# Optimization experiments

Hardware: AMD Instinct MI355X
Metric: run time of the kernel (lower is better)

Reference implementation:

```python
import jax, jax.numpy as jnp
import numpy as np

NC, NG, D = 50000, 3000, 64
E_CG, E_GC, E_GG = 3_000_000, 3_000_000, 100_000
KEEP = 0.9  # 1 - drop_out


def _mask(key, n):
    return (jax.random.uniform(key, (n, 1)) < KEEP).astype(jnp.float32) / KEEP


def setup_inputs() -> dict:
    key = jax.random.key(0)
    ks = jax.random.split(key, 20)
    return {
        "c_feat": jax.random.normal(ks[0], (NC, D), jnp.float32),
        "g_feat": jax.random.normal(ks[1], (NG, D), jnp.float32),
        "cj_cell": jax.random.uniform(ks[2], (NC, 1), jnp.float32),
        "ci_cell": jax.random.uniform(ks[3], (NC, 1), jnp.float32),
        "cj_gene": jax.random.uniform(ks[4], (NG, 1), jnp.float32),
        "ci_gene": jax.random.uniform(ks[5], (NG, 1), jnp.float32),
        "cjj_gene": jax.random.uniform(ks[6], (NG, 1), jnp.float32),
        "cii_gene": jax.random.uniform(ks[7], (NG, 1), jnp.float32),
        "mask_exp": _mask(ks[8], NC),
        "mask_rev": _mask(ks[9], NG),
        "mask_gg": _mask(ks[10], NG),
        "src_cg": jax.random.randint(ks[11], (E_CG,), 0, NC, jnp.int32),
        "dst_cg": jax.random.randint(ks[12], (E_CG,), 0, NG, jnp.int32),
        "src_gc": jax.random.randint(ks[13], (E_GC,), 0, NG, jnp.int32),
        "dst_gc": jax.random.randint(ks[14], (E_GC,), 0, NC, jnp.int32),
        "src_gg": jax.random.randint(ks[15], (E_GG,), 0, NG, jnp.int32),
        "dst_gg": jax.random.randint(ks[16], (E_GG,), 0, NG, jnp.int32),
    }


def _light_conv(src_feats, cj, mask, ci, src, dst, n_dst):
    # weighted_feats = src_feats * dropout(cj); copy_u + sum; scale by ci
    wf = src_feats * (cj * mask)                      # [Nsrc, D]
    agg = jax.ops.segment_sum(wf[src], dst, num_segments=n_dst)  # [Ndst, D]
    return agg * ci


def reference(c_feat, g_feat, cj_cell, ci_cell, cj_gene, ci_gene,
              cjj_gene, cii_gene, mask_exp, mask_rev, mask_gg,
              src_cg, dst_cg, src_gc, dst_gc, src_gg, dst_gg):
    alpha1 = 0.5
    # relation 'exp': cell -> gene
    g_exp = _light_conv(c_feat, cj_cell, mask_exp, ci_gene, src_cg, dst_cg, NG)
    # relation 'reverse-exp': gene -> cell (only relation targeting cells)
    c_out = _light_conv(g_feat, cj_gene, mask_rev, ci_cell, src_gc, dst_gc, NC)
    # relation 'co-exp': gene -> gene (uses cjj/cii)
    g_gg = _light_conv(g_feat, cjj_gene, mask_gg, cii_gene, src_gg, dst_gg, NG)
    # aggregate='stack' over gene dst relations, then alpha-weighted combine
    g_out = alpha1 * g_exp + (1.0 - alpha1) * g_gg
    return (c_out, g_out)
```

## Files before the change

### kernel.cpp

```cpp
#include <hip/hip_runtime.h>

#define NC 50000
#define NG 3000
#define D  64

#define NB_CG 750
#define NB_GC 782
#define PBITS 18
#define TILE  8192
#define NPREP 128
#define CAP   4608
#define GG_CAP 128
#define OVF_CAP 262144

__device__ inline unsigned short f2bf(float x) {
    unsigned u = __float_as_uint(x);
    unsigned r = u + 0x7FFFu + ((u >> 16) & 1u);
    return (unsigned short)(r >> 16);
}

template <bool BF16>
__device__ inline void row8(const void* feat, int s, int l8, float f[8]) {
    if (BF16) {
        const uint4 q = *((const uint4*)((const unsigned short*)feat + (size_t)s * D) + l8);
        f[0] = __uint_as_float(q.x << 16); f[1] = __uint_as_float(q.x & 0xFFFF0000u);
        f[2] = __uint_as_float(q.y << 16); f[3] = __uint_as_float(q.y & 0xFFFF0000u);
        f[4] = __uint_as_float(q.z << 16); f[5] = __uint_as_float(q.z & 0xFFFF0000u);
        f[6] = __uint_as_float(q.w << 16); f[7] = __uint_as_float(q.w & 0xFFFF0000u);
    } else {
        const float4* row = (const float4*)((const float*)feat + (size_t)s * D);
        const float4 a = row[l8];
        const float4 b = row[l8 + 8];
        f[0] = a.x; f[1] = a.y; f[2] = a.z; f[3] = a.w;
        f[4] = b.x; f[5] = b.y; f[6] = b.z; f[7] = b.w;
    }
}


__global__ __launch_bounds__(256) void partition_kernel(
    const int* __restrict__ src_cg, const int* __restrict__ dst_cg, int e_cg, int nt_cg,
    const int* __restrict__ src_gc, const int* __restrict__ dst_gc, int e_gc, int nt_gc,
    const int* __restrict__ src_gg, const int* __restrict__ dst_gg, int e_gg,
    int* __restrict__ cur_cg, int* __restrict__ cur_gc, int* __restrict__ cnt_gg,
    unsigned* __restrict__ bkt_cg, unsigned* __restrict__ bkt_gc, int* __restrict__ bkt_gg,
    int* __restrict__ ovf_cnt, uint2* __restrict__ ovf,
    const float* __restrict__ cj_cell, const float* __restrict__ mask_exp,
    const float* __restrict__ cj_gene, const float* __restrict__ mask_rev,
    const float* __restrict__ cjj_gene, const float* __restrict__ mask_gg,
    float* __restrict__ w_cell, float* __restrict__ w_rev, float* __restrict__ w_gg,
    const float* __restrict__ c_feat, const float* __restrict__ g_feat,
    unsigned short* __restrict__ cf16, unsigned short* __restrict__ gf16, int do_cvt)
{
    const int tid = threadIdx.x;
    const int NT2 = nt_cg + nt_gc;

    if (blockIdx.x >= NT2 + 64) {
        const int pb = blockIdx.x - NT2 - 64;
        const long long stride = (long long)NPREP * 256;
        for (long long i = (long long)pb * 256 + tid; i < NC; i += stride)
            w_cell[i] = cj_cell[i] * mask_exp[i];
        for (long long i = (long long)pb * 256 + tid; i < NG; i += stride) {
            w_rev[i] = cj_gene[i] * mask_rev[i];
            w_gg[i]  = cjj_gene[i] * mask_gg[i];
        }
        if (do_cvt) {
            const long long total8 = (long long)(NC + NG) * D / 8;
            for (long long t = (long long)pb * 256 + tid; t < total8; t += stride) {
                const long long base = t * 8;
                const float* sp; unsigned short* dp;
                if (base < (long long)NC * D) { sp = c_feat + base; dp = cf16 + base; }
                else { sp = g_feat + (base - (long long)NC * D); dp = gf16 + (base - (long long)NC * D); }
                const float4 a = ((const float4*)sp)[0];
                const float4 b = ((const float4*)sp)[1];
                ((ushort4*)dp)[0] = make_ushort4(f2bf(a.x), f2bf(a.y), f2bf(a.z), f2bf(a.w));
                ((ushort4*)dp)[1] = make_ushort4(f2bf(b.x), f2bf(b.y), f2bf(b.z), f2bf(b.w));
            }
        }
        return;
    }

    if (blockIdx.x >= NT2) {
        for (long long e = (long long)(blockIdx.x - NT2) * 256 + tid; e < e_gg;
             e += (long long)64 * 256) {
            const int dd = dst_gg[e];
            const int ss = src_gg[e];
            if ((unsigned)dd >= (unsigned)NG || (unsigned)ss >= (unsigned)NG) continue;
            const int pos = atomicAdd(&cnt_gg[dd], 1);
            if (pos < GG_CAP) bkt_gg[dd * GG_CAP + pos] = ss;
            else {
                const int op = atomicAdd(ovf_cnt, 1);
                if (op >= 0 && op < OVF_CAP)
                    ovf[op] = make_uint2((2u << 30) | (unsigned)ss, (unsigned)dd);
            }
        }
        return;
    }

    const int* src; const int* dst; int ne; int* cur; unsigned* bkt;
    int shift, nbins, t; unsigned rel;
    if (blockIdx.x < nt_cg) { src = src_cg; dst = dst_cg; ne = e_cg; cur = cur_cg; bkt = bkt_cg; shift = 2; nbins = NB_CG; t = blockIdx.x;         rel = 0u; }
    else                    { src = src_gc; dst = dst_gc; ne = e_gc; cur = cur_gc; bkt = bkt_gc; shift = 6; nbins = NB_GC; t = blockIdx.x - nt_cg; rel = 1u; }
    const long long tb = (long long)t * TILE;
    if (tb >= ne) return;
    const int n = (int)((ne - tb) < TILE ? (ne - tb) : TILE);

    __shared__ int th[784];
    __shared__ int toff[784];
    __shared__ int tcur[784];
    __shared__ int gs[784];
    __shared__ unsigned staged[TILE];
    const unsigned PMASK = (1u << PBITS) - 1u;
    const unsigned DMASK = (1u << shift) - 1u;

    for (int i = tid; i < nbins; i += 256) { th[i] = 0; tcur[i] = 0; }
    __syncthreads();
    #pragma unroll 4
    for (int k = 0; k < TILE / 256; ++k) {
        int i = k * 256 + tid;
        if (i < n) {
            unsigned b = ((unsigned)dst[tb + i]) >> shift;
            if (b < (unsigned)nbins) atomicAdd(&th[b], 1);
        }
    }
    __syncthreads();
    if (tid < 64) {
        int carry = 0;
        for (int c = 0; c < nbins; c += 64) {
            int idx = c + tid;
            int v = (idx < nbins) ? th[idx] : 0;
            int incl = v;
            #pragma unroll
            for (int d = 1; d < 64; d <<= 1) {
                int x = __shfl_up(incl, d);
                if (tid >= d) incl += x;
            }
            if (idx < nbins) toff[idx] = incl - v + carry;
            carry += __shfl(incl, 63);
        }
    }
    __syncthreads();
    for (int i = tid; i < nbins; i += 256) {
        const int c = th[i];
        gs[i] = c ? atomicAdd(&cur[i], c) : 0;
    }
    __syncthreads();
    #pragma unroll 4
    for (int k = 0; k < TILE / 256; ++k) {
        int i = k * 256 + tid;
        if (i < n) {
            unsigned d = (unsigned)dst[tb + i];
            unsigned s = (unsigned)src[tb + i];
            unsigned b = d >> shift;
            if (b < (unsigned)nbins) {
                int p = toff[b] + atomicAdd(&tcur[b], 1);
                if (p >= 0 && p < TILE)
                    staged[p] = (b << PBITS) | (s << shift) | (d & DMASK);
            }
        }
    }
    __syncthreads();
    for (int i = tid; i < n; i += 256) {
        const unsigned v = staged[i];
        const unsigned b = v >> PBITS;
        const int local = gs[b] + (i - toff[b]);
        if (local < CAP) {
            bkt[(size_t)b * CAP + local] = v & PMASK;
        } else {
            const unsigned s = (v >> shift) & 0xFFFFu;
            const unsigned dd = (b << shift) | (v & DMASK);
            const int op = atomicAdd(ovf_cnt, 1);
            if (op >= 0 && op < OVF_CAP)
                ovf[op] = make_uint2((rel << 30) | s, dd);
        }
    }
}


template <bool BF16>
__global__ __launch_bounds__(256) void gather3_kernel(
    const unsigned* __restrict__ bkt_cg, const int* __restrict__ cur_cg,
    const unsigned* __restrict__ bkt_gc, const int* __restrict__ cur_gc,
    const void* __restrict__ cfeat, const void* __restrict__ gfeat,
    const float* __restrict__ w_cell, const float* __restrict__ w_rev, const float* __restrict__ w_gg,
    const float* __restrict__ ci_gene, const float* __restrict__ cii_gene, const float* __restrict__ ci_cell,
    const int* __restrict__ cnt_gg, const int* __restrict__ bkt_gg,
    float* __restrict__ g_out, float* __restrict__ c_out)
{
    __shared__ unsigned short sorted[CAP];
    __shared__ int lh[64];
    __shared__ int loff[64];
    __shared__ int lcur[64];

    const bool is_cg = (blockIdx.x < NB_CG);
    const int bin = is_cg ? blockIdx.x : blockIdx.x - NB_CG;
    int n = (is_cg ? cur_cg : cur_gc)[bin];
    n = n > CAP ? CAP : n;
    const long long base = (long long)bin * CAP;
    const unsigned* bkt = is_cg ? bkt_cg : bkt_gc;
    const void* feat = is_cg ? cfeat : gfeat;
    const float* wsrc = is_cg ? w_cell : w_rev;
    const int shift = is_cg ? 2 : 6;
    const int DIVv = is_cg ? 4 : 64;
    const int KPC  = is_cg ? 16 : 1;
    const int tid  = threadIdx.x;
    const int lane = tid & 63;
    const int wid  = tid >> 6;
    const int grp8 = lane >> 3;
    const int l8   = lane & 7;

    for (int i = tid; i < 64; i += 256) { lh[i] = 0; lcur[i] = 0; }
    __syncthreads();
    for (int i = tid; i < n; i += 256) {
        const unsigned v = bkt[base + i];
        const int k = is_cg ? (int)(((v & 3u) << 4) | (((v >> 2) & 0xFFFFu) >> 12))
                            : (int)(v & 63u);
        atomicAdd(&lh[k], 1);
    }
    __syncthreads();
    if (tid < 64) {
        int v = lh[tid];
        int incl = v;
        #pragma unroll
        for (int d = 1; d < 64; d <<= 1) {
            int t = __shfl_up(incl, d);
            if (tid >= d) incl += t;
        }
        loff[tid] = incl - v;
    }
    __syncthreads();
    for (int i = tid; i < n; i += 256) {
        const unsigned v = bkt[base + i];
        const int k = is_cg ? (int)(((v & 3u) << 4) | (((v >> 2) & 0xFFFFu) >> 12))
                            : (int)(v & 63u);
        const int p = loff[k] + atomicAdd(&lcur[k], 1);
        if (p >= 0 && p < CAP) sorted[p] = (unsigned short)((v >> shift) & 0xFFFFu);
    }
    __syncthreads();

    for (int cell = wid; cell < DIVv; cell += 4) {
        const int r = (bin << shift) + cell;
        if (r >= (is_cg ? NG : NC)) continue;

        float fA[8] = {0.f, 0.f, 0.f, 0.f, 0.f, 0.f, 0.f, 0.f};
        {
            const int k0 = cell * KPC, k1 = k0 + KPC - 1;
            const int lo = loff[k0], hi = loff[k1] + lh[k1];
            for (int jj = lo; jj < hi; jj += 16) {
                const int j0 = jj + grp8;
                const int j1 = jj + 8 + grp8;
                const bool v0 = (j0 < hi);
                const bool v1 = (j1 < hi);
                const int s0 = v0 ? (int)sorted[j0] : 0;
                const int s1 = v1 ? (int)sorted[j1] : 0;
                const float w0 = v0 ? wsrc[s0] : 0.0f;
                const float w1 = v1 ? wsrc[s1] : 0.0f;
                float f0[8], f1[8];
                row8<BF16>(feat, s0, l8, f0);
                row8<BF16>(feat, s1, l8, f1);
                #pragma unroll
                for (int q = 0; q < 8; ++q) fA[q] += w0 * f0[q];
                #pragma unroll
                for (int q = 0; q < 8; ++q) fA[q] += w1 * f1[q];
            }
        }

        float fB[8] = {0.f, 0.f, 0.f, 0.f, 0.f, 0.f, 0.f, 0.f};
        if (is_cg) {
            int ngg = cnt_gg[r];
            ngg = ngg > GG_CAP ? GG_CAP : ngg;
            const int* bg = bkt_gg + (size_t)r * GG_CAP;
            for (int jj = 0; jj < ngg; jj += 8) {
                const int j = jj + grp8;
                const bool valid = (j < ngg);
                const int s = valid ? bg[j] : 0;
                const float w = valid ? w_gg[s] : 0.0f;
                float f[8]; row8<BF16>(gfeat, s, l8, f);
                #pragma unroll
                for (int q = 0; q < 8; ++q) fB[q] += w * f[q];
            }
        }

        #pragma unroll
        for (int q = 0; q < 8; ++q) {
            #pragma unroll
            for (int off = 8; off < 64; off <<= 1) fA[q] += __shfl_xor(fA[q], off);
        }
        if (is_cg) {
            #pragma unroll
            for (int q = 0; q < 8; ++q) {
                #pragma unroll
                for (int off = 8; off < 64; off <<= 1) fB[q] += __shfl_xor(fB[q], off);
            }
        }

        if (grp8 == 0) {
            float o[8];
            float* outp;
            if (is_cg) {
                const float sa = 0.5f * ci_gene[r];
                const float sb = 0.5f * cii_gene[r];
                outp = g_out + (size_t)r * D;
                #pragma unroll
                for (int q = 0; q < 8; ++q) o[q] = sa * fA[q] + sb * fB[q];
            } else {
                const float sc = ci_cell[r];
                outp = c_out + (size_t)r * D;
                #pragma unroll
                for (int q = 0; q < 8; ++q) o[q] = sc * fA[q];
            }
            if (BF16) {
                *(float4*)(outp + 8 * l8)     = make_float4(o[0], o[1], o[2], o[3]);
                *(float4*)(outp + 8 * l8 + 4) = make_float4(o[4], o[5], o[6], o[7]);
            } else {
                *(float4*)(outp + 4 * l8)      = make_float4(o[0], o[1], o[2], o[3]);
                *(float4*)(outp + 32 + 4 * l8) = make_float4(o[4], o[5], o[6], o[7]);
            }
        }
    }
}


__global__ __launch_bounds__(256) void ovf_scatter_kernel(
    const int* __restrict__ ovf_cnt, const uint2* __restrict__ ovf,
    const float* __restrict__ c_feat, const float* __restrict__ g_feat,
    const float* __restrict__ w_cell, const float* __restrict__ w_rev, const float* __restrict__ w_gg,
    const float* __restrict__ ci_gene, const float* __restrict__ ci_cell, const float* __restrict__ cii_gene,
    float* __restrict__ c_out, float* __restrict__ g_out)
{
    int cnt = *ovf_cnt;
    cnt = cnt > OVF_CAP ? OVF_CAP : cnt;
    if (cnt <= 0) return;
    const int lane16 = threadIdx.x & 15;
    const int eloc   = threadIdx.x >> 4;
    for (long long e = (long long)blockIdx.x * 16 + eloc; e < cnt;
         e += (long long)gridDim.x * 16) {
        const uint2 v = ovf[e];
        const unsigned rel = v.x >> 30;
        const int s = (int)(v.x & 0x3FFFFFFFu);
        const int d = (int)v.y;
        const float* feat; float* out; float w;
        if (rel == 0u)      { feat = c_feat + (size_t)s * D; out = g_out + (size_t)d * D; w = 0.5f * ci_gene[d] * w_cell[s]; }
        else if (rel == 1u) { feat = g_feat + (size_t)s * D; out = c_out + (size_t)d * D; w = ci_cell[d] * w_rev[s]; }
        else                { feat = g_feat + (size_t)s * D; out = g_out + (size_t)d * D; w = 0.5f * cii_gene[d] * w_gg[s]; }
        const float4 f = *(const float4*)(feat + lane16 * 4);
#if defined(__HIP_DEVICE_COMPILE__)
        unsafeAtomicAdd(out + lane16 * 4 + 0, w * f.x);
        unsafeAtomicAdd(out + lane16 * 4 + 1, w * f.y);
        unsafeAtomicAdd(out + lane16 * 4 + 2, w * f.z);
        unsafeAtomicAdd(out + lane16 * 4 + 3, w * f.w);
#endif
    }
}


__global__ __launch_bounds__(256) void edge_scatter_kernel(
    const float* __restrict__ feat, const float* __restrict__ cj,
    const float* __restrict__ mask, const float* __restrict__ ci,
    const int* __restrict__ src, const int* __restrict__ dst,
    float* __restrict__ out, int nedges, float alpha)
{
    const int lane16 = threadIdx.x & 15;
    const int eloc   = threadIdx.x >> 4;
    const long long e = (long long)blockIdx.x * 16 + eloc;
    if (e >= nedges) return;
    const int s = src[e];
    const int t = dst[e];
    const float w = cj[s] * mask[s] * ci[t] * alpha;
    const float4 v = *(const float4*)(feat + (size_t)s * D + lane16 * 4);
    float* o = out + (size_t)t * D + lane16 * 4;
#if defined(__HIP_DEVICE_COMPILE__)
    unsafeAtomicAdd(o + 0, w * v.x);
    unsafeAtomicAdd(o + 1, w * v.y);
    unsafeAtomicAdd(o + 2, w * v.z);
    unsafeAtomicAdd(o + 3, w * v.w);
#endif
}


extern "C" void kernel_launch(void* const* d_in, const int* in_sizes, int n_in,
                              void* d_out, int out_size, void* d_ws, size_t ws_size,
                              hipStream_t stream)
{
    const float* c_feat   = (const float*)d_in[0];
    const float* g_feat   = (const float*)d_in[1];
    const float* cj_cell  = (const float*)d_in[2];
    const float* ci_cell  = (const float*)d_in[3];
    const float* cj_gene  = (const float*)d_in[4];
    const float* ci_gene  = (const float*)d_in[5];
    const float* cjj_gene = (const float*)d_in[6];
    const float* cii_gene = (const float*)d_in[7];
    const float* mask_exp = (const float*)d_in[8];
    const float* mask_rev = (const float*)d_in[9];
    const float* mask_gg  = (const float*)d_in[10];
    const int*   src_cg   = (const int*)d_in[11];
    const int*   dst_cg   = (const int*)d_in[12];
    const int*   src_gc   = (const int*)d_in[13];
    const int*   dst_gc   = (const int*)d_in[14];
    const int*   src_gg   = (const int*)d_in[15];
    const int*   dst_gg   = (const int*)d_in[16];

    const int e_cg = in_sizes[11];
    const int e_gc = in_sizes[13];
    const int e_gg = in_sizes[15];

    float* c_out = (float*)d_out;
    float* g_out = (float*)d_out + (size_t)NC * D;

    const int nt_cg = (e_cg + TILE - 1) / TILE;
    const int nt_gc = (e_gc + TILE - 1) / TILE;

    int* ws = (int*)d_ws;
    size_t p = 0;
    int* cur_cg  = ws + p; p += NB_CG;
    int* cur_gc  = ws + p; p += NB_GC;
    int* cnt_gg  = ws + p; p += NG;
    int* ovf_cnt = ws + p; p += 1;
    const size_t zcount = p;
    float* w_cell = (float*)(ws + p); p += NC;
    float* w_rev  = (float*)(ws + p); p += NG;
    float* w_gg   = (float*)(ws + p); p += NG;
    unsigned* bkt_cg = (unsigned*)(ws + p); p += (size_t)NB_CG * CAP;
    unsigned* bkt_gc = (unsigned*)(ws + p); p += (size_t)NB_GC * CAP;
    int* bkt_gg = ws + p; p += (size_t)NG * GG_CAP;
    p = (p + 1) & ~(size_t)1;
    uint2* ovf = (uint2*)(ws + p); p += (size_t)OVF_CAP * 2;
    const size_t need_base = p * sizeof(int);
    p = (p + 3) & ~(size_t)3;
    unsigned short* cf16 = (unsigned short*)(ws + p); p += (size_t)NC * D / 2;
    unsigned short* gf16 = (unsigned short*)(ws + p); p += (size_t)NG * D / 2;
    const size_t need_full = p * sizeof(int);

    if (need_base > ws_size || e_cg > 3200000 || e_gc > 3200000 || e_gg > 200000) {
        hipMemsetAsync(d_out, 0, (size_t)out_size * sizeof(float), stream);
        edge_scatter_kernel<<<(e_cg + 15) / 16, 256, 0, stream>>>(
            c_feat, cj_cell, mask_exp, ci_gene, src_cg, dst_cg, g_out, e_cg, 0.5f);
        edge_scatter_kernel<<<(e_gc + 15) / 16, 256, 0, stream>>>(
            g_feat, cj_gene, mask_rev, ci_cell, src_gc, dst_gc, c_out, e_gc, 1.0f);
        edge_scatter_kernel<<<(e_gg + 15) / 16, 256, 0, stream>>>(
            g_feat, cjj_gene, mask_gg, cii_gene, src_gg, dst_gg, g_out, e_gg, 0.5f);
        return;
    }
    const int use_bf16 = (need_full <= ws_size) ? 1 : 0;

    hipMemsetAsync(ws, 0, zcount * sizeof(int), stream);

    partition_kernel<<<nt_cg + nt_gc + 64 + NPREP, 256, 0, stream>>>(
        src_cg, dst_cg, e_cg, nt_cg,
        src_gc, dst_gc, e_gc, nt_gc,
        src_gg, dst_gg, e_gg,
        cur_cg, cur_gc, cnt_gg,
        bkt_cg, bkt_gc, bkt_gg,
        ovf_cnt, ovf,
        cj_cell, mask_exp, cj_gene, mask_rev, cjj_gene, mask_gg,
        w_cell, w_rev, w_gg, c_feat, g_feat, cf16, gf16, use_bf16);

    if (use_bf16) {
        gather3_kernel<true><<<NB_CG + NB_GC, 256, 0, stream>>>(
            bkt_cg, cur_cg, bkt_gc, cur_gc,
            (const void*)cf16, (const void*)gf16,
            w_cell, w_rev, w_gg, ci_gene, cii_gene, ci_cell,
            cnt_gg, bkt_gg, g_out, c_out);
    } else {
        gather3_kernel<false><<<NB_CG + NB_GC, 256, 0, stream>>>(
            bkt_cg, cur_cg, bkt_gc, cur_gc,
            (const void*)c_feat, (const void*)g_feat,
            w_cell, w_rev, w_gg, ci_gene, cii_gene, ci_cell,
            cnt_gg, bkt_gg, g_out, c_out);
    }

    ovf_scatter_kernel<<<64, 256, 0, stream>>>(
        ovf_cnt, ovf, c_feat, g_feat, w_cell, w_rev, w_gg,
        ci_gene, ci_cell, cii_gene, c_out, g_out);
}
```

Baseline: 278.9 us.

## Prescale bf16 features by source weights, unroll gather, fold overflow into gather

The conversion pass now multiplies each source row by its dropout-scaled weight before rounding to bf16, producing separate weighted copies for the reverse and gene-gene relations. Each copy gets an extra zero row that serves as a dummy index. The gather loop therefore needs no per-edge weight lookup or bounds masking and issues four independent row loads per iteration, and launch bounds request higher occupancy. The separate overflow scatter kernel is removed: each output row linearly scans the overflow list before its store. That saves a launch and atomics but costs a read of the overflow counter per block and a full scan per row whenever overflow is nonzero. Rounding now happens after the weighting instead of before.

```diff
diff --git a/kernel.cpp b/kernel.cpp
--- a/kernel.cpp
+++ b/kernel.cpp
@@ -19,21 +19,19 @@
     return (unsigned short)(r >> 16);
 }
 
-template <bool BF16>
-__device__ inline void row8(const void* feat, int s, int l8, float f[8]) {
-    if (BF16) {
-        const uint4 q = *((const uint4*)((const unsigned short*)feat + (size_t)s * D) + l8);
-        f[0] = __uint_as_float(q.x << 16); f[1] = __uint_as_float(q.x & 0xFFFF0000u);
-        f[2] = __uint_as_float(q.y << 16); f[3] = __uint_as_float(q.y & 0xFFFF0000u);
-        f[4] = __uint_as_float(q.z << 16); f[5] = __uint_as_float(q.z & 0xFFFF0000u);
-        f[6] = __uint_as_float(q.w << 16); f[7] = __uint_as_float(q.w & 0xFFFF0000u);
-    } else {
-        const float4* row = (const float4*)((const float*)feat + (size_t)s * D);
-        const float4 a = row[l8];
-        const float4 b = row[l8 + 8];
-        f[0] = a.x; f[1] = a.y; f[2] = a.z; f[3] = a.w;
-        f[4] = b.x; f[5] = b.y; f[6] = b.z; f[7] = b.w;
-    }
+__device__ __forceinline__ void acc8(const uint4& q, float f[8]) {
+    f[0] += __uint_as_float(q.x << 16); f[1] += __uint_as_float(q.x & 0xFFFF0000u);
+    f[2] += __uint_as_float(q.y << 16); f[3] += __uint_as_float(q.y & 0xFFFF0000u);
+    f[4] += __uint_as_float(q.z << 16); f[5] += __uint_as_float(q.z & 0xFFFF0000u);
+    f[6] += __uint_as_float(q.w << 16); f[7] += __uint_as_float(q.w & 0xFFFF0000u);
+}
+
+__device__ inline void row8f(const float* feat, int s, int l8, float f[8]) {
+    const float4* row = (const float4*)(feat + (size_t)s * D);
+    const float4 a = row[l8];
+    const float4 b = row[l8 + 8];
+    f[0] = a.x; f[1] = a.y; f[2] = a.z; f[3] = a.w;
+    f[4] = b.x; f[5] = b.y; f[6] = b.z; f[7] = b.w;
 }
 
 
@@ -49,7 +47,8 @@
     const float* __restrict__ cjj_gene, const float* __restrict__ mask_gg,
     float* __restrict__ w_cell, float* __restrict__ w_rev, float* __restrict__ w_gg,
     const float* __restrict__ c_feat, const float* __restrict__ g_feat,
-    unsigned short* __restrict__ cf16, unsigned short* __restrict__ gf16, int do_cvt)
+    unsigned short* __restrict__ wc16, unsigned short* __restrict__ wg16,
+    unsigned short* __restrict__ wgg16, int do_cvt)
 {
     const int tid = threadIdx.x;
     const int NT2 = nt_cg + nt_gc;
@@ -67,13 +66,33 @@
             const long long total8 = (long long)(NC + NG) * D / 8;
             for (long long t = (long long)pb * 256 + tid; t < total8; t += stride) {
                 const long long base = t * 8;
-                const float* sp; unsigned short* dp;
-                if (base < (long long)NC * D) { sp = c_feat + base; dp = cf16 + base; }
-                else { sp = g_feat + (base - (long long)NC * D); dp = gf16 + (base - (long long)NC * D); }
-                const float4 a = ((const float4*)sp)[0];
-                const float4 b = ((const float4*)sp)[1];
-                ((ushort4*)dp)[0] = make_ushort4(f2bf(a.x), f2bf(a.y), f2bf(a.z), f2bf(a.w));
-                ((ushort4*)dp)[1] = make_ushort4(f2bf(b.x), f2bf(b.y), f2bf(b.z), f2bf(b.w));
+                if (base < (long long)NC * D) {
+                    const int s = (int)(base >> 6);
+                    const float w = cj_cell[s] * mask_exp[s];
+                    const float4 a = ((const float4*)(c_feat + base))[0];
+                    const float4 b = ((const float4*)(c_feat + base))[1];
+                    unsigned short* dp = wc16 + base;
+                    ((ushort4*)dp)[0] = make_ushort4(f2bf(w*a.x), f2bf(w*a.y), f2bf(w*a.z), f2bf(w*a.w));
+                    ((ushort4*)dp)[1] = make_ushort4(f2bf(w*b.x), f2bf(w*b.y), f2bf(w*b.z), f2bf(w*b.w));
+                } else {
+                    const long long gb = base - (long long)NC * D;
+                    const int s = (int)(gb >> 6);
+                    const float wr = cj_gene[s] * mask_rev[s];
+                    const float wg = cjj_gene[s] * mask_gg[s];
+                    const float4 a = ((const float4*)(g_feat + gb))[0];
+                    const float4 b = ((const float4*)(g_feat + gb))[1];
+                    ((ushort4*)(wg16 + gb))[0]  = make_ushort4(f2bf(wr*a.x), f2bf(wr*a.y), f2bf(wr*a.z), f2bf(wr*a.w));
+                    ((ushort4*)(wg16 + gb))[1]  = make_ushort4(f2bf(wr*b.x), f2bf(wr*b.y), f2bf(wr*b.z), f2bf(wr*b.w));
+                    ((ushort4*)(wgg16 + gb))[0] = make_ushort4(f2bf(wg*a.x), f2bf(wg*a.y), f2bf(wg*a.z), f2bf(wg*a.w));
+                    ((ushort4*)(wgg16 + gb))[1] = make_ushort4(f2bf(wg*b.x), f2bf(wg*b.y), f2bf(wg*b.z), f2bf(wg*b.w));
+                }
+            }
+            if (pb == 0) {
+                for (int i = tid; i < D; i += 256) {
+                    wc16[(size_t)NC * D + i] = 0;
+                    wg16[(size_t)NG * D + i] = 0;
+                    wgg16[(size_t)NG * D + i] = 0;
+                }
             }
         }
         return;
@@ -177,13 +196,15 @@
 
 
 template <bool BF16>
-__global__ __launch_bounds__(256) void gather3_kernel(
+__global__ __launch_bounds__(256, 6) void gather3_kernel(
     const unsigned* __restrict__ bkt_cg, const int* __restrict__ cur_cg,
     const unsigned* __restrict__ bkt_gc, const int* __restrict__ cur_gc,
-    const void* __restrict__ cfeat, const void* __restrict__ gfeat,
+    const void* __restrict__ fc, const void* __restrict__ fg, const void* __restrict__ fgg,
+    const float* __restrict__ craw, const float* __restrict__ graw,
     const float* __restrict__ w_cell, const float* __restrict__ w_rev, const float* __restrict__ w_gg,
     const float* __restrict__ ci_gene, const float* __restrict__ cii_gene, const float* __restrict__ ci_cell,
     const int* __restrict__ cnt_gg, const int* __restrict__ bkt_gg,
+    const int* __restrict__ ovf_cnt, const uint2* __restrict__ ovf,
     float* __restrict__ g_out, float* __restrict__ c_out)
 {
     __shared__ unsigned short sorted[CAP];
@@ -197,11 +218,12 @@
     n = n > CAP ? CAP : n;
     const long long base = (long long)bin * CAP;
     const unsigned* bkt = is_cg ? bkt_cg : bkt_gc;
-    const void* feat = is_cg ? cfeat : gfeat;
+    const void* feat = is_cg ? fc : fg;
     const float* wsrc = is_cg ? w_cell : w_rev;
     const int shift = is_cg ? 2 : 6;
     const int DIVv = is_cg ? 4 : 64;
     const int KPC  = is_cg ? 16 : 1;
+    const int DUM  = is_cg ? NC : NG;
     const int tid  = threadIdx.x;
     const int lane = tid & 63;
     const int wid  = tid >> 6;
@@ -237,6 +259,9 @@
     }
     __syncthreads();
 
+    int novf = *ovf_cnt;
+    novf = novf < 0 ? 0 : (novf > OVF_CAP ? OVF_CAP : novf);
+
     for (int cell = wid; cell < DIVv; cell += 4) {
         const int r = (bin << shift) + cell;
         if (r >= (is_cg ? NG : NC)) continue;
@@ -245,22 +270,30 @@
         {
             const int k0 = cell * KPC, k1 = k0 + KPC - 1;
             const int lo = loff[k0], hi = loff[k1] + lh[k1];
-            for (int jj = lo; jj < hi; jj += 16) {
-                const int j0 = jj + grp8;
-                const int j1 = jj + 8 + grp8;
-                const bool v0 = (j0 < hi);
-                const bool v1 = (j1 < hi);
-                const int s0 = v0 ? (int)sorted[j0] : 0;
-                const int s1 = v1 ? (int)sorted[j1] : 0;
-                const float w0 = v0 ? wsrc[s0] : 0.0f;
-                const float w1 = v1 ? wsrc[s1] : 0.0f;
-                float f0[8], f1[8];
-                row8<BF16>(feat, s0, l8, f0);
-                row8<BF16>(feat, s1, l8, f1);
-                #pragma unroll
-                for (int q = 0; q < 8; ++q) fA[q] += w0 * f0[q];
-                #pragma unroll
-                for (int q = 0; q < 8; ++q) fA[q] += w1 * f1[q];
+            if (BF16) {
+                const uint4* fp = (const uint4*)feat;
+                for (int jj = lo; jj < hi; jj += 32) {
+                    const int b0 = jj + grp8;
+                    const int s0 = (b0      < hi) ? (int)sorted[b0]      : DUM;
+                    const int s1 = (b0 + 8  < hi) ? (int)sorted[b0 + 8]  : DUM;
+                    const int s2 = (b0 + 16 < hi) ? (int)sorted[b0 + 16] : DUM;
+                    const int s3 = (b0 + 24 < hi) ? (int)sorted[b0 + 24] : DUM;
+                    const uint4 q0 = fp[(size_t)s0 * 8 + l8];
+                    const uint4 q1 = fp[(size_t)s1 * 8 + l8];
+                    const uint4 q2 = fp[(size_t)s2 * 8 + l8];
+                    const uint4 q3 = fp[(size_t)s3 * 8 + l8];
+                    acc8(q0, fA); acc8(q1, fA); acc8(q2, fA); acc8(q3, fA);
+                }
+            } else {
+                for (int jj = lo; jj < hi; jj += 8) {
+                    const int j = jj + grp8;
+                    const bool valid = (j < hi);
+                    const int s = valid ? (int)sorted[j] : 0;
+                    const float w = valid ? wsrc[s] : 0.0f;
+                    float f[8]; row8f((const float*)feat, s, l8, f);
+                    #pragma unroll
+                    for (int q = 0; q < 8; ++q) fA[q] += w * f[q];
+                }
             }
         }
 
@@ -269,14 +302,27 @@
             int ngg = cnt_gg[r];
             ngg = ngg > GG_CAP ? GG_CAP : ngg;
             const int* bg = bkt_gg + (size_t)r * GG_CAP;
-            for (int jj = 0; jj < ngg; jj += 8) {
-                const int j = jj + grp8;
-                const bool valid = (j < ngg);
-                const int s = valid ? bg[j] : 0;
-                const float w = valid ? w_gg[s] : 0.0f;
-                float f[8]; row8<BF16>(gfeat, s, l8, f);
-                #pragma unroll
-                for (int q = 0; q < 8; ++q) fB[q] += w * f[q];
+            if (BF16) {
+                const uint4* fp = (const uint4*)fgg;
+                for (int jj = 0; jj < ngg; jj += 16) {
+                    const int j0 = jj + grp8;
+                    const int j1 = jj + 8 + grp8;
+                    const int s0 = (j0 < ngg) ? bg[j0] : NG;
+                    const int s1 = (j1 < ngg) ? bg[j1] : NG;
+                    const uint4 q0 = fp[(size_t)s0 * 8 + l8];
+                    const uint4 q1 = fp[(size_t)s1 * 8 + l8];
+                    acc8(q0, fB); acc8(q1, fB);
+                }
+            } else {
+                for (int jj = 0; jj < ngg; jj += 8) {
+                    const int j = jj + grp8;
+                    const bool valid = (j < ngg);
+                    const int s = valid ? bg[j] : 0;
+                    const float w = valid ? w_gg[s] : 0.0f;
+                    float f[8]; row8f(graw, s, l8, f);
+                    #pragma unroll
+                    for (int q = 0; q < 8; ++q) fB[q] += w * f[q];
+                }
             }
         }
 
@@ -297,7 +343,7 @@
             float o[8];
             float* outp;
             if (is_cg) {
-                const float sa = 0.5f * ci_gene[r];
+                const float sa = BF16 ? 0.5f * ci_gene[r] : 0.5f * ci_gene[r];
                 const float sb = 0.5f * cii_gene[r];
                 outp = g_out + (size_t)r * D;
                 #pragma unroll
@@ -308,6 +354,32 @@
                 #pragma unroll
                 for (int q = 0; q < 8; ++q) o[q] = sc * fA[q];
             }
+
+            if (novf > 0) {
+                for (int e = 0; e < novf; ++e) {
+                    const uint2 vv = ovf[e];
+                    const int d = (int)vv.y;
+                    if (d != r) continue;
+                    const unsigned relv = vv.x >> 30;
+                    const int s = (int)(vv.x & 0x3FFFFFFFu);
+                    const float* fr = nullptr; float w = 0.f;
+                    if (is_cg) {
+                        if (relv == 0u && s < NC)      { fr = craw + (size_t)s * D; w = 0.5f * ci_gene[r] * w_cell[s]; }
+                        else if (relv == 2u && s < NG) { fr = graw + (size_t)s * D; w = 0.5f * cii_gene[r] * w_gg[s]; }
+                    } else {
+                        if (relv == 1u && s < NG)      { fr = graw + (size_t)s * D; w = ci_cell[r] * w_rev[s]; }
+                    }
+                    if (fr) {
+                        #pragma unroll
+                        for (int q = 0; q < 8; ++q) {
+                            const int elem = BF16 ? (8 * l8 + q)
+                                                  : (q < 4 ? 4 * l8 + q : 32 + 4 * l8 + (q - 4));
+                            o[q] += w * fr[elem];
+                        }
+                    }
+                }
+            }
+
             if (BF16) {
                 *(float4*)(outp + 8 * l8)     = make_float4(o[0], o[1], o[2], o[3]);
                 *(float4*)(outp + 8 * l8 + 4) = make_float4(o[4], o[5], o[6], o[7]);
@@ -316,39 +388,6 @@
                 *(float4*)(outp + 32 + 4 * l8) = make_float4(o[4], o[5], o[6], o[7]);
             }
         }
-    }
-}
-
-
-__global__ __launch_bounds__(256) void ovf_scatter_kernel(
-    const int* __restrict__ ovf_cnt, const uint2* __restrict__ ovf,
-    const float* __restrict__ c_feat, const float* __restrict__ g_feat,
-    const float* __restrict__ w_cell, const float* __restrict__ w_rev, const float* __restrict__ w_gg,
-    const float* __restrict__ ci_gene, const float* __restrict__ ci_cell, const float* __restrict__ cii_gene,
-    float* __restrict__ c_out, float* __restrict__ g_out)
-{
-    int cnt = *ovf_cnt;
-    cnt = cnt > OVF_CAP ? OVF_CAP : cnt;
-    if (cnt <= 0) return;
-    const int lane16 = threadIdx.x & 15;
-    const int eloc   = threadIdx.x >> 4;
-    for (long long e = (long long)blockIdx.x * 16 + eloc; e < cnt;
-         e += (long long)gridDim.x * 16) {
-        const uint2 v = ovf[e];
-        const unsigned rel = v.x >> 30;
-        const int s = (int)(v.x & 0x3FFFFFFFu);
-        const int d = (int)v.y;
-        const float* feat; float* out; float w;
-        if (rel == 0u)      { feat = c_feat + (size_t)s * D; out = g_out + (size_t)d * D; w = 0.5f * ci_gene[d] * w_cell[s]; }
-        else if (rel == 1u) { feat = g_feat + (size_t)s * D; out = c_out + (size_t)d * D; w = ci_cell[d] * w_rev[s]; }
-        else                { feat = g_feat + (size_t)s * D; out = g_out + (size_t)d * D; w = 0.5f * cii_gene[d] * w_gg[s]; }
-        const float4 f = *(const float4*)(feat + lane16 * 4);
-#if defined(__HIP_DEVICE_COMPILE__)
-        unsafeAtomicAdd(out + lane16 * 4 + 0, w * f.x);
-        unsafeAtomicAdd(out + lane16 * 4 + 1, w * f.y);
-        unsafeAtomicAdd(out + lane16 * 4 + 2, w * f.z);
-        unsafeAtomicAdd(out + lane16 * 4 + 3, w * f.w);
-#endif
     }
 }
 
@@ -426,8 +465,9 @@
     uint2* ovf = (uint2*)(ws + p); p += (size_t)OVF_CAP * 2;
     const size_t need_base = p * sizeof(int);
     p = (p + 3) & ~(size_t)3;
-    unsigned short* cf16 = (unsigned short*)(ws + p); p += (size_t)NC * D / 2;
-    unsigned short* gf16 = (unsigned short*)(ws + p); p += (size_t)NG * D / 2;
+    unsigned short* wc16  = (unsigned short*)(ws + p); p += (size_t)(NC + 1) * D / 2;
+    unsigned short* wg16  = (unsigned short*)(ws + p); p += (size_t)(NG + 1) * D / 2;
+    unsigned short* wgg16 = (unsigned short*)(ws + p); p += (size_t)(NG + 1) * D / 2;
     const size_t need_full = p * sizeof(int);
 
     if (need_base > ws_size || e_cg > 3200000 || e_gc > 3200000 || e_gg > 200000) {
@@ -452,23 +492,21 @@
         bkt_cg, bkt_gc, bkt_gg,
         ovf_cnt, ovf,
         cj_cell, mask_exp, cj_gene, mask_rev, cjj_gene, mask_gg,
-        w_cell, w_rev, w_gg, c_feat, g_feat, cf16, gf16, use_bf16);
+        w_cell, w_rev, w_gg, c_feat, g_feat, wc16, wg16, wgg16, use_bf16);
 
     if (use_bf16) {
         gather3_kernel<true><<<NB_CG + NB_GC, 256, 0, stream>>>(
             bkt_cg, cur_cg, bkt_gc, cur_gc,
-            (const void*)cf16, (const void*)gf16,
+            (const void*)wc16, (const void*)wg16, (const void*)wgg16,
+            c_feat, g_feat,
             w_cell, w_rev, w_gg, ci_gene, cii_gene, ci_cell,
-            cnt_gg, bkt_gg, g_out, c_out);
+            cnt_gg, bkt_gg, ovf_cnt, ovf, g_out, c_out);
     } else {
         gather3_kernel<false><<<NB_CG + NB_GC, 256, 0, stream>>>(
             bkt_cg, cur_cg, bkt_gc, cur_gc,
-            (const void*)c_feat, (const void*)g_feat,
+            (const void*)c_feat, (const void*)g_feat, (const void*)g_feat,
+            c_feat, g_feat,
             w_cell, w_rev, w_gg, ci_gene, cii_gene, ci_cell,
-            cnt_gg, bkt_gg, g_out, c_out);
-    }
-
-    ovf_scatter_kernel<<<64, 256, 0, stream>>>(
-        ovf_cnt, ovf, c_feat, g_feat, w_cell, w_rev, w_gg,
-        ci_gene, ci_cell, cii_gene, c_out, g_out);
-}
+            cnt_gg, bkt_gg, ovf_cnt, ovf, g_out, c_out);
+    }
+}
```

Result: faster. 266.4 us (-4.5%).
